# Performance work log

Measured on AMD Instinct MI355X. Metric: run time of the kernel, lower is better.

Reference implementation:

```python
import jax, jax.numpy as jnp
import numpy as np

D_MODEL = 1024


def setup_inputs() -> dict:
    key = jax.random.key(0)
    k_x, k_qkv, k_proj, k_b = jax.random.split(key, 4)
    b, t, d = 4, 2048, D_MODEL
    scale = 1.0 / np.sqrt(d)
    x = jax.random.normal(k_x, (b, t, d), dtype=jnp.float32)
    # torch Linear(d, 3d, bias=False): weight [3d, d]; we store transposed [d, 3d]
    w_qkv = jax.random.normal(k_qkv, (d, 3 * d), dtype=jnp.float32) * scale
    w_proj = jax.random.normal(k_proj, (d, d), dtype=jnp.float32) * scale
    b_proj = jax.random.normal(k_b, (d,), dtype=jnp.float32) * scale
    return {"x": x, "w_qkv": w_qkv, "w_proj": w_proj, "b_proj": b_proj}


def reference(x, w_qkv, w_proj, b_proj):
    b, t, d = x.shape
    qkv = jnp.einsum("btd,de->bte", x, w_qkv)  # [b, t, 3d]
    q, k, v = jnp.split(qkv, 3, axis=-1)
    att = jnp.einsum("btd,bsd->bts", q, k) / jnp.sqrt(jnp.float32(d))  # [b, t, t]
    causal = jnp.tril(jnp.ones((t, t), dtype=bool))
    att = jnp.where(causal, att, -jnp.inf)
    att = jax.nn.softmax(att, axis=-1)
    out = jnp.einsum("bts,bsd->btd", att, v)
    return jnp.einsum("btd,de->bte", out, w_proj) + b_proj
```

## Files before the change

kernel.cpp:

```cpp
#include <hip/hip_runtime.h>


typedef __bf16 bf16x8_t __attribute__((ext_vector_type(8)));
typedef float  f32x16_t __attribute__((ext_vector_type(16)));
typedef unsigned short u16;

struct alignas(8) u16x4 { u16 x, y, z, w; };

__device__ inline float bf2f(u16 u) {
  union { unsigned u; float f; } c; c.u = ((unsigned)u) << 16; return c.f;
}
__device__ inline u16 f2bf(float f) {
  union { float f; unsigned u; } c; c.f = f;
  unsigned r = c.u + 0x7fffu + ((c.u >> 16) & 1u);
  return (u16)(r >> 16);
}

template<int OUTMODE, int GRIDMODE>
__global__ __launch_bounds__(256, 4)
void gemm_bt(const u16* __restrict__ A, const u16* __restrict__ B,
             void* __restrict__ Cv, u16* __restrict__ C2,
             const float* __restrict__ bias,
             int K, int lda, int ldb, int ldc,
             long sA, long sB, long sC)
{
  int bn0, bm0;
  if (GRIDMODE == 1) {
    const int x = blockIdx.x;
    int r = (int)((sqrtf(8.f * x + 1.f) - 1.f) * 0.5f);
    while ((r + 1) * (r + 2) / 2 <= x) ++r;
    while (r * (r + 1) / 2 > x) --r;
    bm0 = r * 128;
    bn0 = (x - r * (r + 1) / 2) * 128;
  } else if (GRIDMODE == 2) {
    bn0 = blockIdx.x * 128;
    bm0 = ((int)gridDim.y - 1 - (int)blockIdx.y) * 128;
  } else {
    bn0 = blockIdx.x * 128;
    bm0 = blockIdx.y * 128;
  }
  const long bz = blockIdx.z;
  const u16* Ab = A + bz * sA;
  const u16* Bb = B + bz * sB;
  const int Keff = (GRIDMODE == 2) ? min(K, bm0 + 128) : K;

  __shared__ __align__(16) u16 lA[128 * 64];
  __shared__ __align__(16) u16 lB[128 * 64];

  const int tid  = threadIdx.x;
  const int lane = tid & 63;
  const int wv   = tid >> 6;
  const int wm   = (wv >> 1) << 6;
  const int wn   = (wv & 1) << 6;
  const int ml   = lane & 31;
  const int kh   = lane >> 5;
  const int swz  = ml & 7;

  f32x16_t acc[2][2];
#pragma unroll
  for (int i = 0; i < 2; ++i)
#pragma unroll
    for (int j = 0; j < 2; ++j)
#pragma unroll
      for (int r = 0; r < 16; ++r)
        acc[i][j][r] = 0.f;

  const long ldA2 = (long)lda * 2, ldB2 = (long)ldb * 2;
  const int rowA = tid >> 3;
  const int csw  = (tid & 7) ^ (rowA & 7);
  const char* pA = (const char*)(Ab + (long)bm0 * lda) + (long)rowA * ldA2 + (csw << 4);
  const char* pB = (const char*)(Bb + (long)bn0 * ldb) + (long)rowA * ldB2 + (csw << 4);
  const int ldsbo = tid * 16;

  for (int k0 = 0; k0 < Keff; k0 += 64) {
    const long kb = (long)k0 * 2;
#pragma unroll
    for (int r = 0; r < 4; ++r)
      __builtin_amdgcn_global_load_lds(
          (const __attribute__((address_space(1))) unsigned int*)(pA + kb + (long)(r * 32) * ldA2),
          (__attribute__((address_space(3))) unsigned int*)((char*)lA + ldsbo + r * 4096), 16, 0, 0);
#pragma unroll
    for (int r = 0; r < 4; ++r)
      __builtin_amdgcn_global_load_lds(
          (const __attribute__((address_space(1))) unsigned int*)(pB + kb + (long)(r * 32) * ldB2),
          (__attribute__((address_space(3))) unsigned int*)((char*)lB + ldsbo + r * 4096), 16, 0, 0);
    __syncthreads();

#pragma unroll
    for (int s = 0; s < 4; ++s) {
      const int ck = ((s * 2 + kh) ^ swz) << 3;
      bf16x8_t a0 = *(const bf16x8_t*)&lA[(wm + ml) * 64 + ck];
      bf16x8_t a1 = *(const bf16x8_t*)&lA[(wm + 32 + ml) * 64 + ck];
      bf16x8_t b0 = *(const bf16x8_t*)&lB[(wn + ml) * 64 + ck];
      bf16x8_t b1 = *(const bf16x8_t*)&lB[(wn + 32 + ml) * 64 + ck];
      acc[0][0] = __builtin_amdgcn_mfma_f32_32x32x16_bf16(a0, b0, acc[0][0], 0, 0, 0);
      acc[0][1] = __builtin_amdgcn_mfma_f32_32x32x16_bf16(a0, b1, acc[0][1], 0, 0, 0);
      acc[1][0] = __builtin_amdgcn_mfma_f32_32x32x16_bf16(a1, b0, acc[1][0], 0, 0, 0);
      acc[1][1] = __builtin_amdgcn_mfma_f32_32x32x16_bf16(a1, b1, acc[1][1], 0, 0, 0);
    }
    __syncthreads();
  }

  if (OUTMODE == 2 && bn0 >= 2048) {
#pragma unroll
    for (int i = 0; i < 2; ++i) {
#pragma unroll
      for (int g = 0; g < 4; ++g) {
        const int rowb = bm0 + wm + i * 32 + g * 8 + kh * 4;
        const int b_  = rowb >> 11;
        const int s_  = rowb & 2047;
#pragma unroll
        for (int j = 0; j < 2; ++j) {
          const int dcol = bn0 - 2048 + wn + j * 32 + ml;
          u16x4 o = {f2bf(acc[i][j][g * 4 + 0]), f2bf(acc[i][j][g * 4 + 1]),
                     f2bf(acc[i][j][g * 4 + 2]), f2bf(acc[i][j][g * 4 + 3])};
          *(u16x4*)&C2[(((long)b_ * 1024 + dcol) << 11) + s_] = o;
        }
      }
    }
    return;
  }
  u16*   Cb16 = (u16*)Cv + bz * sC;
  float* Cf32 = (float*)Cv + bz * sC;
#pragma unroll
  for (int i = 0; i < 2; ++i) {
#pragma unroll
    for (int j = 0; j < 2; ++j) {
#pragma unroll
      for (int reg = 0; reg < 16; ++reg) {
        const int row = bm0 + wm + i * 32 + (reg & 3) + 8 * (reg >> 2) + kh * 4;
        const int col = bn0 + wn + j * 32 + ml;
        float v = acc[i][j][reg];
        if (OUTMODE == 1) {
          Cf32[(long)row * ldc + col] = v + bias[col];
        } else {
          Cb16[(long)row * ldc + col] = f2bf(v);
        }
      }
    }
  }
}

__global__ __launch_bounds__(256)
void cvt_f32_bf16(const float* __restrict__ in, u16* __restrict__ out) {
  const int i = blockIdx.x * 256 + threadIdx.x;
  float4 v = ((const float4*)in)[i];
  u16x4 o = {f2bf(v.x), f2bf(v.y), f2bf(v.z), f2bf(v.w)};
  ((u16x4*)out)[i] = o;
}

__global__ __launch_bounds__(256)
void transpose_weights(const float* __restrict__ wqkv, u16* __restrict__ wqkvT,
                       const float* __restrict__ wproj, u16* __restrict__ wprojT) {
  const bool isq = blockIdx.x < 96;
  const float* in = isq ? wqkv : wproj;
  u16* out        = isq ? wqkvT : wprojT;
  const int C     = isq ? 3072 : 1024;
  const int c0 = (isq ? blockIdx.x : (blockIdx.x - 96)) * 32;
  const int r0 = blockIdx.y * 32;
  __shared__ float t[32][33];
  const int tx = threadIdx.x & 31, ty = threadIdx.x >> 5;
#pragma unroll
  for (int i = 0; i < 32; i += 8)
    t[ty + i][tx] = in[(long)(r0 + ty + i) * C + (c0 + tx)];
  __syncthreads();
#pragma unroll
  for (int i = 0; i < 32; i += 8)
    out[(long)(c0 + ty + i) * 1024 + (r0 + tx)] = f2bf(t[tx][ty + i]);
}

__global__ __launch_bounds__(256)
void softmax_causal(u16* __restrict__ SP) {
  const int t = blockIdx.x;
  const int b = blockIdx.y;
  u16* row = SP + ((long)b * 2048 + t) * 2048;
  const int len = t + 1;
  const int end = ((t >> 7) + 1) << 7;
  const int tid = threadIdx.x;
  const int s0  = tid * 8;
  const float scale = 0.03125f;
  __shared__ float red[8];

  float v[8];
  float lmax = -3.0e38f;
  if (s0 < end) {
    u16x4 u0 = *(const u16x4*)(row + s0);
    u16x4 u1 = *(const u16x4*)(row + s0 + 4);
    v[0] = bf2f(u0.x); v[1] = bf2f(u0.y); v[2] = bf2f(u0.z); v[3] = bf2f(u0.w);
    v[4] = bf2f(u1.x); v[5] = bf2f(u1.y); v[6] = bf2f(u1.z); v[7] = bf2f(u1.w);
#pragma unroll
    for (int e = 0; e < 8; ++e)
      if (s0 + e < len) { v[e] *= scale; lmax = fmaxf(lmax, v[e]); }
  }
#pragma unroll
  for (int o = 32; o; o >>= 1) lmax = fmaxf(lmax, __shfl_down(lmax, o));
  if ((tid & 63) == 0) red[tid >> 6] = lmax;
  __syncthreads();
  const float m = fmaxf(fmaxf(red[0], red[1]), fmaxf(red[2], red[3]));

  float lsum = 0.f;
  if (s0 < len) {
#pragma unroll
    for (int e = 0; e < 8; ++e)
      if (s0 + e < len) { v[e] = __expf(v[e] - m); lsum += v[e]; }
  }
#pragma unroll
  for (int o = 32; o; o >>= 1) lsum += __shfl_down(lsum, o);
  if ((tid & 63) == 0) red[4 + (tid >> 6)] = lsum;
  __syncthreads();
  const float inv = 1.0f / (red[4] + red[5] + red[6] + red[7]);

  if (s0 < end) {
    u16x4 o0, o1;
#pragma unroll
    for (int e = 0; e < 8; ++e) {
      const float ve = (s0 + e < len) ? v[e] * inv : 0.f;
      if (e < 4) ((u16*)&o0)[e] = f2bf(ve);
      else       ((u16*)&o1)[e - 4] = f2bf(ve);
    }
    *(u16x4*)(row + s0)     = o0;
    *(u16x4*)(row + s0 + 4) = o1;
  }
}

extern "C" void kernel_launch(void* const* d_in, const int* in_sizes, int n_in,
                              void* d_out, int out_size, void* d_ws, size_t ws_size,
                              hipStream_t stream) {
  (void)in_sizes; (void)n_in; (void)out_size; (void)ws_size;
  const float* x      = (const float*)d_in[0];
  const float* w_qkv  = (const float*)d_in[1];
  const float* w_proj = (const float*)d_in[2];
  const float* b_proj = (const float*)d_in[3];
  float* y = (float*)d_out;
  char*  ws = (char*)d_ws;

  u16* xbf    = (u16*)(ws);
  u16* qk     = (u16*)(ws + (16l << 20));
  u16* wqkvT  = (u16*)(ws + (48l << 20));
  u16* wprojT = (u16*)(ws + (54l << 20));
  u16* vT     = (u16*)(ws + (56l << 20));
  u16* SP     = (u16*)(ws + (72l << 20));
  u16* attn   = xbf;

  cvt_f32_bf16<<<8192, 256, 0, stream>>>(x, xbf);
  transpose_weights<<<dim3(128, 32), 256, 0, stream>>>(w_qkv, wqkvT, w_proj, wprojT);
  gemm_bt<2, 0><<<dim3(24, 64, 1), 256, 0, stream>>>(
      xbf, wqkvT, qk, vT, nullptr, 1024, 1024, 1024, 2048, 0, 0, 0);
  gemm_bt<0, 1><<<dim3(136, 1, 4), 256, 0, stream>>>(
      qk, qk + 1024, SP, nullptr, nullptr, 1024, 2048, 2048, 2048,
      (long)2048 * 2048, (long)2048 * 2048, (long)2048 * 2048);
  softmax_causal<<<dim3(2048, 4), 256, 0, stream>>>(SP);
  gemm_bt<0, 2><<<dim3(8, 16, 4), 256, 0, stream>>>(
      SP, vT, attn, nullptr, nullptr, 2048, 2048, 2048, 1024,
      (long)2048 * 2048, (long)1024 * 2048, (long)2048 * 1024);
  gemm_bt<1, 0><<<dim3(8, 64, 1), 256, 0, stream>>>(
      attn, wprojT, y, nullptr, b_proj, 1024, 1024, 1024, 1024, 0, 0, 0);
}
```

Baseline: 285.4 us.

## Fuse causal softmax into QK^T and PV GEMM epilogues with atomic row sums

Removes the standalone softmax kernel. The QK^T GEMM epilogue now writes exp(score*scale) with the causal mask applied on diagonal tiles, and accumulates per-row sums into a global buffer with atomics. The PV GEMM epilogue divides by those row sums. This avoids one full read and write pass over the score matrix and one launch, at the cost of atomics, a memset, and dropping the max-subtraction (overflow risk for large-magnitude scores). Occupancy hint raised from 4 to 5 blocks per CU.

```diff
diff --git a/kernel.cpp b/kernel.cpp
--- a/kernel.cpp
+++ b/kernel.cpp
@@ -17,10 +17,10 @@
 }
 
 template<int OUTMODE, int GRIDMODE>
-__global__ __launch_bounds__(256, 4)
+__global__ __launch_bounds__(256, 5)
 void gemm_bt(const u16* __restrict__ A, const u16* __restrict__ B,
              void* __restrict__ Cv, u16* __restrict__ C2,
-             const float* __restrict__ bias,
+             const float* __restrict__ bias, float* __restrict__ rs,
              int K, int lda, int ldb, int ldc,
              long sA, long sB, long sC)
 {
@@ -101,44 +101,111 @@
     __syncthreads();
   }
 
-  if (OUTMODE == 2 && bn0 >= 2048) {
+  if (OUTMODE == 2) {
+    if (bn0 >= 2048) {
+#pragma unroll
+      for (int i = 0; i < 2; ++i) {
+#pragma unroll
+        for (int g = 0; g < 4; ++g) {
+          const int rowb = bm0 + wm + i * 32 + g * 8 + kh * 4;
+          const int b_  = rowb >> 11;
+          const int s_  = rowb & 2047;
+#pragma unroll
+          for (int j = 0; j < 2; ++j) {
+            const int dcol = bn0 - 2048 + wn + j * 32 + ml;
+            u16x4 o = {f2bf(acc[i][j][g * 4 + 0]), f2bf(acc[i][j][g * 4 + 1]),
+                       f2bf(acc[i][j][g * 4 + 2]), f2bf(acc[i][j][g * 4 + 3])};
+            *(u16x4*)&C2[(((long)b_ * 1024 + dcol) << 11) + s_] = o;
+          }
+        }
+      }
+    } else {
+      u16* Cb16 = (u16*)Cv;
+#pragma unroll
+      for (int i = 0; i < 2; ++i)
+#pragma unroll
+        for (int j = 0; j < 2; ++j)
+#pragma unroll
+          for (int reg = 0; reg < 16; ++reg) {
+            const int row = bm0 + wm + i * 32 + (reg & 3) + 8 * (reg >> 2) + kh * 4;
+            const int col = bn0 + wn + j * 32 + ml;
+            Cb16[(long)row * ldc + col] = f2bf(acc[i][j][reg]);
+          }
+    }
+    return;
+  }
+
+  if (OUTMODE == 3) {
+    const float scale = 0.03125f;
+    const bool diag = (bm0 == bn0);
+    u16* Cb16 = (u16*)Cv + bz * sC;
+    float* rsb = rs + bz * 2048;
+    float ev[2][16];
 #pragma unroll
     for (int i = 0; i < 2; ++i) {
 #pragma unroll
-      for (int g = 0; g < 4; ++g) {
-        const int rowb = bm0 + wm + i * 32 + g * 8 + kh * 4;
-        const int b_  = rowb >> 11;
-        const int s_  = rowb & 2047;
+      for (int reg = 0; reg < 16; ++reg) {
+        const int rl   = wm + i * 32 + (reg & 3) + 8 * (reg >> 2) + kh * 4;
+        const int grow = bm0 + rl;
+        float rsum = 0.f;
 #pragma unroll
         for (int j = 0; j < 2; ++j) {
-          const int dcol = bn0 - 2048 + wn + j * 32 + ml;
-          u16x4 o = {f2bf(acc[i][j][g * 4 + 0]), f2bf(acc[i][j][g * 4 + 1]),
-                     f2bf(acc[i][j][g * 4 + 2]), f2bf(acc[i][j][g * 4 + 3])};
-          *(u16x4*)&C2[(((long)b_ * 1024 + dcol) << 11) + s_] = o;
-        }
+          const int col = bn0 + wn + j * 32 + ml;
+          float e = (diag && col > grow) ? 0.f : __expf(acc[i][j][reg] * scale);
+          Cb16[(long)grow * ldc + col] = f2bf(e);
+          rsum += e;
+        }
+        ev[i][reg] = rsum;
       }
     }
+#pragma unroll
+    for (int m = 1; m < 32; m <<= 1)
+#pragma unroll
+      for (int i = 0; i < 2; ++i)
+#pragma unroll
+        for (int reg = 0; reg < 16; ++reg)
+          ev[i][reg] += __shfl_xor(ev[i][reg], m);
+    if (ml == 0) {
+#pragma unroll
+      for (int i = 0; i < 2; ++i)
+#pragma unroll
+        for (int reg = 0; reg < 16; ++reg) {
+          const int grow = bm0 + wm + i * 32 + (reg & 3) + 8 * (reg >> 2) + kh * 4;
+          atomicAdd(&rsb[grow], ev[i][reg]);
+        }
+    }
     return;
   }
-  u16*   Cb16 = (u16*)Cv + bz * sC;
+
+  if (OUTMODE == 4) {
+    float* rsl = (float*)lA;
+    if (tid < 128) rsl[tid] = 1.0f / rs[bz * 2048 + bm0 + tid];
+    __syncthreads();
+    u16* Cb16 = (u16*)Cv + bz * sC;
+#pragma unroll
+    for (int i = 0; i < 2; ++i)
+#pragma unroll
+      for (int j = 0; j < 2; ++j)
+#pragma unroll
+        for (int reg = 0; reg < 16; ++reg) {
+          const int rl  = wm + i * 32 + (reg & 3) + 8 * (reg >> 2) + kh * 4;
+          const int col = bn0 + wn + j * 32 + ml;
+          Cb16[(long)(bm0 + rl) * ldc + col] = f2bf(acc[i][j][reg] * rsl[rl]);
+        }
+    return;
+  }
+
   float* Cf32 = (float*)Cv + bz * sC;
 #pragma unroll
-  for (int i = 0; i < 2; ++i) {
-#pragma unroll
-    for (int j = 0; j < 2; ++j) {
+  for (int i = 0; i < 2; ++i)
+#pragma unroll
+    for (int j = 0; j < 2; ++j)
 #pragma unroll
       for (int reg = 0; reg < 16; ++reg) {
         const int row = bm0 + wm + i * 32 + (reg & 3) + 8 * (reg >> 2) + kh * 4;
         const int col = bn0 + wn + j * 32 + ml;
-        float v = acc[i][j][reg];
-        if (OUTMODE == 1) {
-          Cf32[(long)row * ldc + col] = v + bias[col];
-        } else {
-          Cb16[(long)row * ldc + col] = f2bf(v);
-        }
+        Cf32[(long)row * ldc + col] = acc[i][j][reg] + bias[col];
       }
-    }
-  }
 }
 
 __global__ __launch_bounds__(256)
@@ -169,60 +236,6 @@
     out[(long)(c0 + ty + i) * 1024 + (r0 + tx)] = f2bf(t[tx][ty + i]);
 }
 
-__global__ __launch_bounds__(256)
-void softmax_causal(u16* __restrict__ SP) {
-  const int t = blockIdx.x;
-  const int b = blockIdx.y;
-  u16* row = SP + ((long)b * 2048 + t) * 2048;
-  const int len = t + 1;
-  const int end = ((t >> 7) + 1) << 7;
-  const int tid = threadIdx.x;
-  const int s0  = tid * 8;
-  const float scale = 0.03125f;
-  __shared__ float red[8];
-
-  float v[8];
-  float lmax = -3.0e38f;
-  if (s0 < end) {
-    u16x4 u0 = *(const u16x4*)(row + s0);
-    u16x4 u1 = *(const u16x4*)(row + s0 + 4);
-    v[0] = bf2f(u0.x); v[1] = bf2f(u0.y); v[2] = bf2f(u0.z); v[3] = bf2f(u0.w);
-    v[4] = bf2f(u1.x); v[5] = bf2f(u1.y); v[6] = bf2f(u1.z); v[7] = bf2f(u1.w);
-#pragma unroll
-    for (int e = 0; e < 8; ++e)
-      if (s0 + e < len) { v[e] *= scale; lmax = fmaxf(lmax, v[e]); }
-  }
-#pragma unroll
-  for (int o = 32; o; o >>= 1) lmax = fmaxf(lmax, __shfl_down(lmax, o));
-  if ((tid & 63) == 0) red[tid >> 6] = lmax;
-  __syncthreads();
-  const float m = fmaxf(fmaxf(red[0], red[1]), fmaxf(red[2], red[3]));
-
-  float lsum = 0.f;
-  if (s0 < len) {
-#pragma unroll
-    for (int e = 0; e < 8; ++e)
-      if (s0 + e < len) { v[e] = __expf(v[e] - m); lsum += v[e]; }
-  }
-#pragma unroll
-  for (int o = 32; o; o >>= 1) lsum += __shfl_down(lsum, o);
-  if ((tid & 63) == 0) red[4 + (tid >> 6)] = lsum;
-  __syncthreads();
-  const float inv = 1.0f / (red[4] + red[5] + red[6] + red[7]);
-
-  if (s0 < end) {
-    u16x4 o0, o1;
-#pragma unroll
-    for (int e = 0; e < 8; ++e) {
-      const float ve = (s0 + e < len) ? v[e] * inv : 0.f;
-      if (e < 4) ((u16*)&o0)[e] = f2bf(ve);
-      else       ((u16*)&o1)[e - 4] = f2bf(ve);
-    }
-    *(u16x4*)(row + s0)     = o0;
-    *(u16x4*)(row + s0 + 4) = o1;
-  }
-}
-
 extern "C" void kernel_launch(void* const* d_in, const int* in_sizes, int n_in,
                               void* d_out, int out_size, void* d_ws, size_t ws_size,
                               hipStream_t stream) {
@@ -239,20 +252,21 @@
   u16* wqkvT  = (u16*)(ws + (48l << 20));
   u16* wprojT = (u16*)(ws + (54l << 20));
   u16* vT     = (u16*)(ws + (56l << 20));
-  u16* SP     = (u16*)(ws + (72l << 20));
+  u16* E      = (u16*)(ws + (72l << 20));
+  float* rsum = (float*)(ws + (104l << 20));
   u16* attn   = xbf;
 
+  hipMemsetAsync(rsum, 0, 4 * 2048 * sizeof(float), stream);
   cvt_f32_bf16<<<8192, 256, 0, stream>>>(x, xbf);
   transpose_weights<<<dim3(128, 32), 256, 0, stream>>>(w_qkv, wqkvT, w_proj, wprojT);
   gemm_bt<2, 0><<<dim3(24, 64, 1), 256, 0, stream>>>(
-      xbf, wqkvT, qk, vT, nullptr, 1024, 1024, 1024, 2048, 0, 0, 0);
-  gemm_bt<0, 1><<<dim3(136, 1, 4), 256, 0, stream>>>(
-      qk, qk + 1024, SP, nullptr, nullptr, 1024, 2048, 2048, 2048,
+      xbf, wqkvT, qk, vT, nullptr, nullptr, 1024, 1024, 1024, 2048, 0, 0, 0);
+  gemm_bt<3, 1><<<dim3(136, 1, 4), 256, 0, stream>>>(
+      qk, qk + 1024, E, nullptr, nullptr, rsum, 1024, 2048, 2048, 2048,
       (long)2048 * 2048, (long)2048 * 2048, (long)2048 * 2048);
-  softmax_causal<<<dim3(2048, 4), 256, 0, stream>>>(SP);
-  gemm_bt<0, 2><<<dim3(8, 16, 4), 256, 0, stream>>>(
-      SP, vT, attn, nullptr, nullptr, 2048, 2048, 2048, 1024,
+  gemm_bt<4, 2><<<dim3(8, 16, 4), 256, 0, stream>>>(
+      E, vT, attn, nullptr, nullptr, rsum, 2048, 2048, 2048, 1024,
       (long)2048 * 2048, (long)1024 * 2048, (long)2048 * 1024);
   gemm_bt<1, 0><<<dim3(8, 64, 1), 256, 0, stream>>>(
-      attn, wprojT, y, nullptr, b_proj, 1024, 1024, 1024, 1024, 0, 0, 0);
-}
+      attn, wprojT, y, nullptr, b_proj, nullptr, 1024, 1024, 1024, 1024, 0, 0, 0);
+}
```

New measurement: 345.7 us. 21.1% more time.
